# Optimization experiments

Measured on AMD Instinct MI355X. Metric: run time of the kernel, lower is better.

## Reference

```python
import jax, jax.numpy as jnp
import numpy as np

EPS = 1e-7
KERNELS = ((5, 5), (7, 1), (1, 7))
SCALES = (60, 30, 15, 8)


def avg_pool(x, kh, kw):
    # PyTorch AvgPool2d(kernel, stride=1, padding=(kh//2, kw//2)), count_include_pad=True
    s = jax.lax.reduce_window(x, 0.0, jax.lax.add, (1, 1, kh, kw), (1, 1, 1, 1),
                              ((0, 0), (0, 0), (kh // 2, kh // 2), (kw // 2, kw // 2)))
    return s / (kh * kw)


def resize_bilinear(x, oh, ow):
    # F.interpolate(mode='bilinear', align_corners=True), NCHW
    B, C, H, W = x.shape
    def coords(o, s):
        pos = jnp.arange(o) * ((s - 1) / max(o - 1, 1))
        i0 = jnp.floor(pos).astype(jnp.int32)
        i1 = jnp.minimum(i0 + 1, s - 1)
        w = (pos - i0).astype(x.dtype)
        return w, i0, i1
    wy, y0, y1 = coords(oh, H)
    wx, x0, x1 = coords(ow, W)
    rows = x[:, :, y0, :] * (1 - wy)[None, None, :, None] + x[:, :, y1, :] * wy[None, None, :, None]
    return rows[:, :, :, x0] * (1 - wx) + rows[:, :, :, x1] * wx


def setup_inputs() -> dict:
    key = jax.random.key(0)
    ks = jax.random.split(key, 12)
    B, C, H, shot = 2, 1024, 60, 1
    hid, tdim = 256, 300
    return {
        "weight": jax.random.uniform(ks[0], (B, shot, 1, 1), dtype=jnp.float32),
        "query_feat_4": jax.random.normal(ks[1], (B, C, H, H), dtype=jnp.float32),
        "supp_feats": jax.random.normal(ks[2], (shot, B, C, H, H), dtype=jnp.float32),
        "masks": jax.random.uniform(ks[3], (shot, B, 1, 473, 473), dtype=jnp.float32),
        "k": jax.random.normal(ks[4], (B, hid, H, H), dtype=jnp.float32),
        "text": jax.random.normal(ks[5], (B, tdim), dtype=jnp.float32),
        "prototype": jax.random.normal(ks[6], (B, hid, 1, 1), dtype=jnp.float32),
        "w_q": jax.random.normal(ks[7], (tdim + hid, hid), dtype=jnp.float32) * 0.05,
        "w_k": jax.random.normal(ks[8], (hid, hid), dtype=jnp.float32) * 0.05,
        "w_bl": jax.random.normal(ks[9], (hid, hid), dtype=jnp.float32) * 0.05,
        "w_proj": jax.random.normal(ks[10], (hid, hid), dtype=jnp.float32) * 0.05,
        "b_proj": jnp.zeros((hid,), dtype=jnp.float32),
    }


def reference(weight, query_feat_4, supp_feats, masks, k, text, prototype, w_q, w_k, w_bl, w_proj, b_proj):
    # ---------------- SPM: self-activation prior mask ----------------
    B, C, H, W = query_feat_4.shape
    S = H * W
    # pooled query features per kernel (shared across supports)
    q_pooled = []
    for (kh, kw) in KERNELS:
        tq = avg_pool(query_feat_4, kh, kw).reshape(B, C, S)
        tq_t = jnp.transpose(tq, (0, 2, 1))                    # [B,S,C]
        qn = jnp.sqrt((tq_t ** 2).sum(-1, keepdims=True))      # [B,S,1]
        q_pooled.append((tq_t, qn))

    corr_list = []
    for i in range(supp_feats.shape[0]):  # loop over shot (small, fixed)
        tmp_mask = resize_bilinear(masks[i], H, W)
        s = supp_feats[i] * tmp_mask
        region = []
        for (kh, kw), (tq_t, qn) in zip(KERNELS, q_pooled):
            ts = avg_pool(s, kh, kw).reshape(B, C, S)          # [B,C,S]
            sn = jnp.sqrt((ts ** 2).sum(1, keepdims=True))     # [B,1,S]
            sim = jnp.matmul(tq_t, ts) / (jnp.matmul(qn, sn) + EPS) * qn  # [B,S,S]
            sim = sim.mean(2)                                  # [B,S]
            mn = sim.min(1, keepdims=True)
            mx = sim.max(1, keepdims=True)
            sim = (sim - mn) / (mx - mn + EPS)
            region.append(sim.reshape(B, H, W))
        corr_list.append(jnp.stack(region, 1).mean(1))         # [B,H,W]
    corr = jnp.stack(corr_list, 1)                             # [B,shot,H,W]
    corr1 = (weight * corr).sum(1, keepdims=True)              # [B,1,H,W]
    corr2 = resize_bilinear(corr1, SCALES[1], SCALES[1])
    corr3 = resize_bilinear(corr1, SCALES[2], SCALES[2])
    corr4 = resize_bilinear(corr1, SCALES[3], SCALES[3])

    # ---------------- APA: bi-linear cross-modal attention ----------------
    Bk, hid, h, w = k.shape
    proto = prototype.reshape(Bk, 1, hid)                      # [B,1,hid]
    q = jnp.concatenate([text[:, None, :], proto], axis=-1)    # [B,1,embed]
    kx = jnp.einsum('oi,bihw->bohw', w_k, k).reshape(Bk, hid, h * w)
    kx = jnp.transpose(kx, (0, 2, 1))                          # [B,S,hid]
    qx = jnp.einsum('bqe,eh->bqh', q, w_q)                     # [B,1,hid]
    qw = jnp.einsum('bqh,hd->bqd', qx, w_bl)                   # bi_linear score
    score = jnp.einsum('bqd,bsd->bqs', qw, kx)                 # [B,1,S]
    score = jax.nn.softmax(score, axis=-1)
    out = jnp.einsum('bqs,bsd->bqd', score, kx)
    out = jnp.einsum('bqd,do->bqo', out, w_proj) + b_proj      # proj (dropout=eval no-op)
    out = out + proto
    return corr1, corr2, corr3, corr4, out
```

## Files before the change

kernel.cpp:

```cpp
#include <hip/hip_runtime.h>
#include <math.h>

#define EPSF 1e-7f
#define Bsz 2
#define Cch 1024
#define Hh 60
#define Ssz 3600
#define HID 256
#define TDIM 300
#define MH 473

#define TROWS 15
#define LROWS 21
#define LPITCH 68
#define CPG 8

#define OFF_SN2    0
#define OFF_DOT    21600
#define OFF_WMAP   43200
#define OFF_V      64800
#define OFF_NORM   70944
#define OFF_SCORE  92544
#define OFF_KBAR   99744
#define OFF_U      100256

__global__ void __launch_bounds__(256) k_pool_sn2(const float* __restrict__ supp,
                                                  const float* __restrict__ masks,
                                                  const float* __restrict__ text,
                                                  const float* __restrict__ proto,
                                                  const float* __restrict__ w_q,
                                                  const float* __restrict__ w_bl,
                                                  const float* __restrict__ w_k,
                                                  float* __restrict__ ws) {
    __shared__ float  mk[LROWS * LPITCH];
    __shared__ float4 raw[LROWS * LPITCH];
    __shared__ float4 h5s[LROWS * LPITCH];
    int tid = threadIdx.x;
    int tile = blockIdx.x;
    int cg = blockIdx.y;
    int b = blockIdx.z;
    int y0 = tile * TROWS;

    if (cg == 128) {
        if (tile != 0) return;
        char* smem = (char*)raw;
        int lane = tid & 63, wv = tid >> 6;
        float4* p4  = (float4*)smem;
        float*  pf  = (float*)smem;
        float*  xs  = (float*)(smem + 4096);
        float*  qxs = (float*)(smem + 6400);
        float*  qws = (float*)(smem + 7424);
        const float4* wq4  = (const float4*)w_q;
        const float4* wbl4 = (const float4*)w_bl;
        const float4* wk4  = (const float4*)w_k;

        #pragma unroll
        for (int j = 0; j < 3; ++j) {
            int e = tid + 256 * j;
            if (e < TDIM) xs[e] = text[b * TDIM + e];
            else if (e < TDIM + HID) xs[e] = proto[b * HID + e - TDIM];
        }
        __syncthreads();
        float4 acc = {0.f, 0.f, 0.f, 0.f};
        #pragma unroll 4
        for (int j = 0; j < 139; ++j) {
            int e = wv + 4 * j;
            if (e < TDIM + HID) {
                float x = xs[e];
                float4 f = wq4[(size_t)e * 64 + lane];
                acc.x += x * f.x; acc.y += x * f.y; acc.z += x * f.z; acc.w += x * f.w;
            }
        }
        p4[wv * 64 + lane] = acc;
        __syncthreads();
        qxs[tid] = pf[tid] + pf[256 + tid] + pf[512 + tid] + pf[768 + tid];
        __syncthreads();

        acc.x = acc.y = acc.z = acc.w = 0.f;
        #pragma unroll 4
        for (int j = 0; j < 64; ++j) {
            int e = wv + 4 * j;
            float x = qxs[e];
            float4 f = wbl4[(size_t)e * 64 + lane];
            acc.x += x * f.x; acc.y += x * f.y; acc.z += x * f.z; acc.w += x * f.w;
        }
        p4[wv * 64 + lane] = acc;
        __syncthreads();
        qws[tid] = pf[tid] + pf[256 + tid] + pf[512 + tid] + pf[768 + tid];
        __syncthreads();

        acc.x = acc.y = acc.z = acc.w = 0.f;
        #pragma unroll 4
        for (int j = 0; j < 64; ++j) {
            int e = wv + 4 * j;
            float x = qws[e];
            float4 f = wk4[(size_t)e * 64 + lane];
            acc.x += x * f.x; acc.y += x * f.y; acc.z += x * f.z; acc.w += x * f.w;
        }
        p4[wv * 64 + lane] = acc;
        __syncthreads();
        ws[OFF_U + b * HID + tid] = pf[tid] + pf[256 + tid] + pf[512 + tid] + pf[768 + tid];
        return;
    }

    const float4 z4 = {0.f, 0.f, 0.f, 0.f};
    for (int i = tid; i < LROWS * LPITCH; i += 256) {
        mk[i] = 0.f; raw[i] = z4; h5s[i] = z4;
    }
    __syncthreads();

    int lr[5], lx[5]; bool lv[5], la[5];
    #pragma unroll
    for (int j = 0; j < 5; ++j) {
        int idx = tid + 256 * j;
        int r = idx / 60, x = idx - 60 * r;
        lr[j] = r; lx[j] = x;
        la[j] = idx < 1260;
        int iy = y0 - 3 + r;
        lv[j] = la[j] && (iy >= 0) && (iy < Hh);
    }
    #pragma unroll
    for (int j = 0; j < 5; ++j)
        if (lv[j]) {
            int iy = y0 - 3 + lr[j];
            mk[lr[j] * LPITCH + 4 + lx[j]] =
                masks[(size_t)b * MH * MH + (size_t)(iy * 8) * MH + lx[j] * 8];
        }

    int orow[4], ox[4]; bool ov[4];
    #pragma unroll
    for (int j = 0; j < 4; ++j) {
        int o = tid + 256 * j;
        int oy = o / 60, x = o - 60 * oy;
        orow[j] = oy + 3; ox[j] = x; ov[j] = o < 900;
    }
    float a0[4] = {0,0,0,0}, a1[4] = {0,0,0,0}, a2[4] = {0,0,0,0};

    const float* chbase = supp + ((size_t)b * Cch + (size_t)cg * CPG) * Ssz + (y0 - 3) * 60;
    float4 pf[5];
    #pragma unroll
    for (int j = 0; j < 5; ++j) {
        int idx = tid + 256 * j;
        pf[j] = z4;
        if (lv[j]) {
            pf[j].x = chbase[idx];
            pf[j].y = chbase[Ssz + idx];
            pf[j].z = chbase[2 * Ssz + idx];
            pf[j].w = chbase[3 * Ssz + idx];
        }
    }

    for (int p = 0; p < 2; ++p) {
        __syncthreads();
        #pragma unroll
        for (int j = 0; j < 5; ++j)
            if (lv[j]) {
                float m = mk[lr[j] * LPITCH + 4 + lx[j]];
                float4 v = pf[j];
                raw[lr[j] * LPITCH + 4 + lx[j]] =
                    make_float4(v.x * m, v.y * m, v.z * m, v.w * m);
            }
        __syncthreads();
        #pragma unroll
        for (int j = 0; j < 5; ++j)
            if (la[j]) {
                int base = lr[j] * LPITCH + 4 + lx[j];
                float4 m2 = raw[base - 2], m1 = raw[base - 1];
                float4 c0 = raw[base], p1 = raw[base + 1], p2 = raw[base + 2];
                float4 h5;
                h5.x = m2.x + m1.x + c0.x + p1.x + p2.x;
                h5.y = m2.y + m1.y + c0.y + p1.y + p2.y;
                h5.z = m2.z + m1.z + c0.z + p1.z + p2.z;
                h5.w = m2.w + m1.w + c0.w + p1.w + p2.w;
                h5s[base] = h5;
            }
        __syncthreads();
        if (p == 0) {
            const float* nb = chbase + (size_t)4 * Ssz;
            #pragma unroll
            for (int j = 0; j < 5; ++j) {
                int idx = tid + 256 * j;
                pf[j] = z4;
                if (lv[j]) {
                    pf[j].x = nb[idx];
                    pf[j].y = nb[Ssz + idx];
                    pf[j].z = nb[2 * Ssz + idx];
                    pf[j].w = nb[3 * Ssz + idx];
                }
            }
        }
        #pragma unroll
        for (int j = 0; j < 4; ++j)
            if (ov[j]) {
                int base = orow[j] * LPITCH + 4 + ox[j];
                float4 sa = h5s[base - 2*LPITCH], sb = h5s[base - LPITCH], sc0 = h5s[base];
                float4 sd = h5s[base + LPITCH], se = h5s[base + 2*LPITCH];
                float p55x = (sa.x + sb.x + sc0.x + sd.x + se.x) * (1.f / 25.f);
                float p55y = (sa.y + sb.y + sc0.y + sd.y + se.y) * (1.f / 25.f);
                float p55z = (sa.z + sb.z + sc0.z + sd.z + se.z) * (1.f / 25.f);
                float p55w = (sa.w + sb.w + sc0.w + sd.w + se.w) * (1.f / 25.f);
                float4 ra = raw[base - 3*LPITCH], rb = raw[base - 2*LPITCH], rc = raw[base - LPITCH];
                float4 rd = raw[base], re = raw[base + LPITCH], rf = raw[base + 2*LPITCH], rg = raw[base + 3*LPITCH];
                float p71x = (ra.x + rb.x + rc.x + rd.x + re.x + rf.x + rg.x) * (1.f / 7.f);
                float p71y = (ra.y + rb.y + rc.y + rd.y + re.y + rf.y + rg.y) * (1.f / 7.f);
                float p71z = (ra.z + rb.z + rc.z + rd.z + re.z + rf.z + rg.z) * (1.f / 7.f);
                float p71w = (ra.w + rb.w + rc.w + rd.w + re.w + rf.w + rg.w) * (1.f / 7.f);
                float4 m3o = raw[base - 3], p3o = raw[base + 3];
                float p17x = (sc0.x + m3o.x + p3o.x) * (1.f / 7.f);
                float p17y = (sc0.y + m3o.y + p3o.y) * (1.f / 7.f);
                float p17z = (sc0.z + m3o.z + p3o.z) * (1.f / 7.f);
                float p17w = (sc0.w + m3o.w + p3o.w) * (1.f / 7.f);
                a0[j] += p55x * p55x + p55y * p55y + p55z * p55z + p55w * p55w;
                a1[j] += p71x * p71x + p71y * p71y + p71z * p71z + p71w * p71w;
                a2[j] += p17x * p17x + p17y * p17y + p17z * p17z + p17w * p17w;
            }
    }
    float* acc = ws + OFF_SN2 + (size_t)(b * 3) * Ssz;
    #pragma unroll
    for (int j = 0; j < 4; ++j)
        if (ov[j]) {
            int q = (y0 + orow[j] - 3) * 60 + ox[j];
            atomicAdd(&acc[q], a0[j]);
            atomicAdd(&acc[Ssz + q], a1[j]);
            atomicAdd(&acc[2 * Ssz + q], a2[j]);
        }
}

__global__ void __launch_bounds__(1024) k_wmap(const float* __restrict__ masks,
                                               float* __restrict__ ws) {
    __shared__ float inv[LROWS * LPITCH];
    int tile = blockIdx.x;
    int bk = blockIdx.y;
    int b = bk / 3, kt = bk % 3;
    int tid = threadIdx.x;
    int y0 = tile * TROWS;
    for (int i = tid; i < LROWS * LPITCH; i += 1024) inv[i] = 0.f;
    __syncthreads();
    const float* pp = ws + OFF_SN2 + (size_t)bk * Ssz;
    #pragma unroll
    for (int j = 0; j < 2; ++j) {
        int idx = tid + 1024 * j;
        if (idx < 1260) {
            int r = idx / 60, x = idx - 60 * r;
            int iy = y0 - 3 + r;
            if (iy >= 0 && iy < Hh) {
                int q = iy * 60 + x;
                float s = pp[q];
                inv[r * LPITCH + 4 + x] = 1.0f / sqrtf(fmaxf(s, 1e-30f));
            }
        }
    }
    __syncthreads();
    int kh = (kt == 0) ? 5 : (kt == 1) ? 7 : 1;
    int kw = (kt == 0) ? 5 : (kt == 2) ? 7 : 1;
    int rh = kh / 2, rw = kw / 2;
    float norm = 1.f / (float)(kh * kw);
    int o = tid;
    if (o < 900) {
        int oy = o / 60, x = o - 60 * oy;
        int base = (oy + 3) * LPITCH + 4 + x;
        float s = 0.f;
        for (int dy = -rh; dy <= rh; ++dy)
            for (int dx = -rw; dx <= rw; ++dx)
                s += inv[base + dy * LPITCH + dx];
        int gy = y0 + oy;
        float m = masks[(size_t)b * MH * MH + (size_t)(gy * 8) * MH + x * 8];
        ws[OFF_WMAP + (size_t)bk * Ssz + gy * 60 + x] = s * norm * m;
    }
}

__global__ void k_v(const float* __restrict__ supp, float* __restrict__ ws) {
    int cB = blockIdx.x, b = blockIdx.y;
    int tid = threadIdx.x, lane = tid & 63, w = tid >> 6;
    int c0 = cB * 4;
    const float4* sp4 = (const float4*)(supp + ((size_t)b * Cch + c0) * Ssz);
    const float4* w04 = (const float4*)(ws + OFF_WMAP + (size_t)(b * 3 + 0) * Ssz);
    const float4* w14 = (const float4*)(ws + OFF_WMAP + (size_t)(b * 3 + 1) * Ssz);
    const float4* w24 = (const float4*)(ws + OFF_WMAP + (size_t)(b * 3 + 2) * Ssz);
    float a[4][3];
    #pragma unroll
    for (int cc = 0; cc < 4; ++cc) { a[cc][0] = 0; a[cc][1] = 0; a[cc][2] = 0; }
    #pragma unroll
    for (int j = 0; j < 4; ++j) {
        int idx = tid + 256 * j;
        if (idx < 900) {
            float4 g0 = w04[idx], g1 = w14[idx], g2 = w24[idx];
            #pragma unroll
            for (int cc = 0; cc < 4; ++cc) {
                float4 f = sp4[cc * 900 + idx];
                a[cc][0] += f.x * g0.x + f.y * g0.y + f.z * g0.z + f.w * g0.w;
                a[cc][1] += f.x * g1.x + f.y * g1.y + f.z * g1.z + f.w * g1.w;
                a[cc][2] += f.x * g2.x + f.y * g2.y + f.z * g2.z + f.w * g2.w;
            }
        }
    }
    #pragma unroll
    for (int m = 32; m >= 1; m >>= 1)
        #pragma unroll
        for (int cc = 0; cc < 4; ++cc) {
            a[cc][0] += __shfl_xor(a[cc][0], m, 64);
            a[cc][1] += __shfl_xor(a[cc][1], m, 64);
            a[cc][2] += __shfl_xor(a[cc][2], m, 64);
        }
    __shared__ float r[4][3][4];
    if (lane == 0)
        #pragma unroll
        for (int cc = 0; cc < 4; ++cc) {
            r[cc][0][w] = a[cc][0]; r[cc][1][w] = a[cc][1]; r[cc][2][w] = a[cc][2];
        }
    __syncthreads();
    if (tid < 12) {
        int cc = tid / 3, kk = tid - cc * 3;
        float s = r[cc][kk][0] + r[cc][kk][1] + r[cc][kk][2] + r[cc][kk][3];
        ws[OFF_V + (size_t)(b * 3 + kk) * Cch + c0 + cc] = s;
    }
}

__global__ void k_dot(const float* __restrict__ query, float* __restrict__ ws) {
    int qt = blockIdx.x, cc = blockIdx.y, b = blockIdx.z;
    int q = qt * 256 + threadIdx.x;
    if (q >= Ssz) return;
    const float* v0 = ws + OFF_V + (size_t)(b * 3 + 0) * Cch;
    const float* v1 = ws + OFF_V + (size_t)(b * 3 + 1) * Cch;
    const float* v2 = ws + OFF_V + (size_t)(b * 3 + 2) * Cch;
    float a0 = 0, a1 = 0, a2 = 0;
    int c0 = cc * 64;
    #pragma unroll 8
    for (int c = c0; c < c0 + 64; ++c) {
        float qv = query[((size_t)b * Cch + c) * Ssz + q];
        a0 += qv * v0[c]; a1 += qv * v1[c]; a2 += qv * v2[c];
    }
    float* dst = ws + OFF_DOT + (size_t)(b * 3) * Ssz + q;
    atomicAdd(&dst[0], a0);
    atomicAdd(&dst[Ssz], a1);
    atomicAdd(&dst[2 * Ssz], a2);
}

__global__ void __launch_bounds__(1024) k_sim(float* __restrict__ ws) {
    int bkx = blockIdx.x;
    int tid = threadIdx.x;
    int lane = tid & 63, w = tid >> 6;

    __shared__ float sA[66 * LPITCH];
    __shared__ float sB[66 * LPITCH];
    __shared__ float rmin[16], rmax[16];
    int bk = bkx; int b = bk / 3; int kt = bk % 3;

    const float* dp0 = ws + OFF_DOT + (size_t)(b * 3 + kt) * Ssz;
    for (int i = tid; i < 66 * LPITCH; i += 1024) {
        int r = i / LPITCH, col = i - r * LPITCH;
        int y = r - 3, x = col - 4;
        float s = 0.f;
        if (y >= 0 && y < Hh && x >= 0 && x < Hh) {
            s = dp0[y * Hh + x];
        }
        sA[i] = s;
    }
    __syncthreads();
    if (kt != 1) {
        for (int idx = tid; idx < 66 * 60; idx += 1024) {
            int r = idx / 60, x = idx - 60 * r;
            int base = r * LPITCH + 4 + x;
            if (kt == 0)
                sB[base] = sA[base - 2] + sA[base - 1] + sA[base] + sA[base + 1] + sA[base + 2];
            else
                sB[base] = sA[base - 3] + sA[base - 2] + sA[base - 1] + sA[base]
                         + sA[base + 1] + sA[base + 2] + sA[base + 3];
        }
    }
    __syncthreads();
    float norm = ((kt == 0) ? (1.f / 25.f) : (1.f / 7.f)) * (1.f / (float)Ssz);
    float vals[4];
    float vmin = INFINITY, vmax = -INFINITY;
    #pragma unroll
    for (int j = 0; j < 4; ++j) {
        int q = tid + j * 1024;
        if (q < Ssz) {
            int y = q / Hh, x = q - y * Hh;
            int base = (y + 3) * LPITCH + 4 + x;
            float s;
            if (kt == 0)
                s = sB[base - 2*LPITCH] + sB[base - LPITCH] + sB[base]
                  + sB[base + LPITCH] + sB[base + 2*LPITCH];
            else if (kt == 1)
                s = sA[base - 3*LPITCH] + sA[base - 2*LPITCH] + sA[base - LPITCH]
                  + sA[base] + sA[base + LPITCH] + sA[base + 2*LPITCH] + sA[base + 3*LPITCH];
            else
                s = sB[base];
            float val = s * norm;
            vals[j] = val;
            vmin = fminf(vmin, val); vmax = fmaxf(vmax, val);
        }
    }
    #pragma unroll
    for (int m = 32; m >= 1; m >>= 1) {
        vmin = fminf(vmin, __shfl_xor(vmin, m, 64));
        vmax = fmaxf(vmax, __shfl_xor(vmax, m, 64));
    }
    if (lane == 0) { rmin[w] = vmin; rmax[w] = vmax; }
    __syncthreads();
    float mn = rmin[0], mx = rmax[0];
    #pragma unroll
    for (int ww = 1; ww < 16; ++ww) {
        mn = fminf(mn, rmin[ww]); mx = fmaxf(mx, rmax[ww]);
    }
    float inv = 1.f / (mx - mn + EPSF);
    float* np = ws + OFF_NORM + (size_t)(b * 3 + kt) * Ssz;
    #pragma unroll
    for (int j = 0; j < 4; ++j) {
        int q = tid + j * 1024;
        if (q < Ssz) np[q] = (vals[j] - mn) * inv;
    }
}

__global__ void __launch_bounds__(1024)
k_score(const float* __restrict__ kin, const float* __restrict__ weight,
        float* __restrict__ ws, float* __restrict__ out) {
    int st = blockIdx.x, b = blockIdx.y;
    int tid = threadIdx.x;

    if (st == 29) {
        __shared__ float sF[Ssz];
        float wq3 = weight[b] * (1.f / 3.f);
        const float* n0 = ws + OFF_NORM + (size_t)(b * 3 + 0) * Ssz;
        const float* n1 = ws + OFF_NORM + (size_t)(b * 3 + 1) * Ssz;
        const float* n2 = ws + OFF_NORM + (size_t)(b * 3 + 2) * Ssz;
        #pragma unroll
        for (int j = 0; j < 4; ++j) {
            int q = tid + j * 1024;
            if (q < Ssz) {
                float s = n0[q] + n1[q] + n2[q];
                sF[q] = s;
                out[b * Ssz + q] = wq3 * s;
            }
        }
        __syncthreads();
        #pragma unroll
        for (int j = 0; j < 2; ++j) {
            int o = tid + j * 1024;
            if (o >= 1189) continue;
            int O, p, outi;
            if (o < 900)       { O = 30; p = o;        outi = 7200 + b * 900 + p; }
            else if (o < 1125) { O = 15; p = o - 900;  outi = 9000 + b * 225 + p; }
            else               { O = 8;  p = o - 1125; outi = 9450 + b * 64 + p; }
            int y = p / O, x = p - y * O;
            float sc = 59.f / (float)(O - 1);
            float py = y * sc, px = x * sc;
            int y0 = (int)floorf(py), x0 = (int)floorf(px);
            int y1 = min(y0 + 1, 59), x1 = min(x0 + 1, 59);
            float wy = py - y0, wx = px - x0;
            float v = sF[y0 * 60 + x0] * (1.f - wy) * (1.f - wx)
                    + sF[y1 * 60 + x0] * wy * (1.f - wx)
                    + sF[y0 * 60 + x1] * (1.f - wy) * wx
                    + sF[y1 * 60 + x1] * wy * wx;
            out[outi] = wq3 * v;
        }
        return;
    }

    __shared__ float us[HID];
    __shared__ float part[8][128];
    if (tid < HID) us[tid] = ws[OFF_U + b * HID + tid];
    __syncthreads();
    int sl = tid & 127, pt = tid >> 7;
    int s = st * 128 + sl;
    float a = 0.f;
    if (s < Ssz) {
        const float* kb = kin + ((size_t)b * HID + pt * 32) * Ssz + s;
        const float* up = us + pt * 32;
        #pragma unroll
        for (int i = 0; i < 32; ++i) a += up[i] * kb[(size_t)i * Ssz];
    }
    part[pt][sl] = a;
    __syncthreads();
    if (tid < 128 && st * 128 + tid < Ssz) {
        float t = 0.f;
        #pragma unroll
        for (int p = 0; p < 8; ++p) t += part[p][tid];
        ws[OFF_SCORE + (size_t)b * Ssz + st * 128 + tid] = t;
    }
}

__global__ void k_kbar(const float* __restrict__ kin, float* __restrict__ ws) {
    int i = blockIdx.x, b = blockIdx.y;
    int tid = threadIdx.x;
    int lane = tid & 63, w = tid >> 6;
    __shared__ float r1[4], r2[4];
    const float4* s4 = (const float4*)(ws + OFF_SCORE + (size_t)b * Ssz);
    float4 sv[4]; bool act[4];
    float mx = -INFINITY;
    #pragma unroll
    for (int j = 0; j < 4; ++j) {
        int idx = tid + 256 * j;
        act[j] = idx < 900;
        if (act[j]) {
            float4 v = s4[idx];
            sv[j] = v;
            mx = fmaxf(mx, fmaxf(fmaxf(v.x, v.y), fmaxf(v.z, v.w)));
        }
    }
    #pragma unroll
    for (int m = 32; m >= 1; m >>= 1) mx = fmaxf(mx, __shfl_xor(mx, m, 64));
    if (lane == 0) r1[w] = mx;
    __syncthreads();
    mx = fmaxf(fmaxf(r1[0], r1[1]), fmaxf(r1[2], r1[3]));
    __syncthreads();
    const float4* kr = (const float4*)(kin + ((size_t)b * HID + i) * Ssz);
    float se = 0.f, wsum = 0.f;
    #pragma unroll
    for (int j = 0; j < 4; ++j) {
        if (act[j]) {
            int idx = tid + 256 * j;
            float4 v = sv[j];
            float ex = expf(v.x - mx), ey = expf(v.y - mx);
            float ez = expf(v.z - mx), ew = expf(v.w - mx);
            se += ex + ey + ez + ew;
            float4 k4 = kr[idx];
            wsum += ex * k4.x + ey * k4.y + ez * k4.z + ew * k4.w;
        }
    }
    #pragma unroll
    for (int m = 32; m >= 1; m >>= 1) {
        se += __shfl_xor(se, m, 64);
        wsum += __shfl_xor(wsum, m, 64);
    }
    if (lane == 0) { r1[w] = se; r2[w] = wsum; }
    __syncthreads();
    if (tid == 0) {
        float seT = r1[0] + r1[1] + r1[2] + r1[3];
        float wsT = r2[0] + r2[1] + r2[2] + r2[3];
        ws[OFF_KBAR + b * HID + i] = wsT / seT;
    }
}

__global__ void __launch_bounds__(1024, 1)
k_apa_out(const float* __restrict__ w_k, const float* __restrict__ w_proj,
          const float* __restrict__ b_proj, const float* __restrict__ proto,
          const float* __restrict__ ws, float* __restrict__ out) {
    int b = blockIdx.x;
    int tid = threadIdx.x;
    int lane = tid & 63, w = tid >> 6;
    __shared__ float4 kbs[64];
    __shared__ float o1s[256];
    __shared__ float4 p4[16][64];
    const float4* wk4 = (const float4*)w_k;
    const float4* wp4 = (const float4*)w_proj;

    if (tid < 64) kbs[tid] = ((const float4*)(ws + OFF_KBAR + b * HID))[tid];
    __syncthreads();

    float4 kb4 = kbs[lane];
    #pragma unroll
    for (int r = 0; r < 16; ++r) {
        int h = w + 16 * r;
        float4 f = wk4[(size_t)h * 64 + lane];
        float p = f.x * kb4.x + f.y * kb4.y + f.z * kb4.z + f.w * kb4.w;
        #pragma unroll
        for (int m = 32; m >= 1; m >>= 1) p += __shfl_xor(p, m, 64);
        if (lane == 0) o1s[h] = p;
    }
    __syncthreads();

    float4 acc = {0.f, 0.f, 0.f, 0.f};
    #pragma unroll
    for (int j = 0; j < 16; ++j) {
        int d = w + 16 * j;
        float x = o1s[d];
        float4 f = wp4[(size_t)d * 64 + lane];
        acc.x += x * f.x; acc.y += x * f.y; acc.z += x * f.z; acc.w += x * f.w;
    }
    p4[w][lane] = acc;
    __syncthreads();
    if (tid < 256) {
        const float* pf = (const float*)p4;
        float s = 0.f;
        #pragma unroll
        for (int ww = 0; ww < 16; ++ww) s += pf[ww * 256 + tid];
        out[9578 + b * HID + tid] = s + b_proj[tid] + proto[b * HID + tid];
    }
}

extern "C" void kernel_launch(void* const* d_in, const int* in_sizes, int n_in,
                              void* d_out, int out_size, void* d_ws, size_t ws_size,
                              hipStream_t stream) {
    const float* weight = (const float*)d_in[0];
    const float* query  = (const float*)d_in[1];
    const float* supp   = (const float*)d_in[2];
    const float* masks  = (const float*)d_in[3];
    const float* kin    = (const float*)d_in[4];
    const float* text   = (const float*)d_in[5];
    const float* proto  = (const float*)d_in[6];
    const float* w_q    = (const float*)d_in[7];
    const float* w_k    = (const float*)d_in[8];
    const float* w_bl   = (const float*)d_in[9];
    const float* w_proj = (const float*)d_in[10];
    const float* b_proj = (const float*)d_in[11];
    float* out = (float*)d_out;
    float* ws  = (float*)d_ws;

    hipMemsetAsync(ws, 0, (size_t)(2 * 6 * Ssz) * sizeof(float), stream);

    k_pool_sn2<<<dim3(4, 129, 2), 256, 0, stream>>>(supp, masks, text, proto,
                                                    w_q, w_bl, w_k, ws);
    k_wmap<<<dim3(4, 6), 1024, 0, stream>>>(masks, ws);
    k_v<<<dim3(256, 2), 256, 0, stream>>>(supp, ws);
    k_dot<<<dim3(15, 16, 2), 256, 0, stream>>>(query, ws);
    k_sim<<<6, 1024, 0, stream>>>(ws);
    k_score<<<dim3(30, 2), 1024, 0, stream>>>(kin, weight, ws, out);
    k_kbar<<<dim3(HID, 2), 256, 0, stream>>>(kin, ws);
    k_apa_out<<<Bsz, 1024, 0, stream>>>(w_k, w_proj, b_proj, proto, ws, out);
}
```

Baseline: 224.3 us.

## Split serial APA query matvec chain across three kernels with atomic partial sums

The chain of three matrix-vector products (w_q, w_bl, w_k) used to run in one block per batch inside the pool kernel. It is now split across k_pool_sn2, k_wmap and k_v. Each stage is spread over several blocks that write partial sums with atomicAdd into new zeroed workspace slots, so one long serial block no longer sets the pool kernel's tail. The cost is a larger memset, extra atomics, and the qx and qw intermediates passing through global memory between kernels.

```diff
diff --git a/kernel.cpp b/kernel.cpp
--- a/kernel.cpp
+++ b/kernel.cpp
@@ -17,91 +17,43 @@
 
 #define OFF_SN2    0
 #define OFF_DOT    21600
-#define OFF_WMAP   43200
-#define OFF_V      64800
-#define OFF_NORM   70944
-#define OFF_SCORE  92544
-#define OFF_KBAR   99744
-#define OFF_U      100256
+#define OFF_QX     43200
+#define OFF_QW     43712
+#define OFF_U      44224
+#define ZERO_END   44736
+#define OFF_WMAP   44736
+#define OFF_V      66336
+#define OFF_NORM   72480
+#define OFF_SCORE  94080
+#define OFF_KBAR   101280
 
 __global__ void __launch_bounds__(256) k_pool_sn2(const float* __restrict__ supp,
                                                   const float* __restrict__ masks,
                                                   const float* __restrict__ text,
                                                   const float* __restrict__ proto,
                                                   const float* __restrict__ w_q,
-                                                  const float* __restrict__ w_bl,
-                                                  const float* __restrict__ w_k,
                                                   float* __restrict__ ws) {
     __shared__ float  mk[LROWS * LPITCH];
     __shared__ float4 raw[LROWS * LPITCH];
     __shared__ float4 h5s[LROWS * LPITCH];
     int tid = threadIdx.x;
     int tile = blockIdx.x;
-    int cg = blockIdx.y;
     int b = blockIdx.z;
     int y0 = tile * TROWS;
 
-    if (cg == 128) {
-        if (tile != 0) return;
-        char* smem = (char*)raw;
-        int lane = tid & 63, wv = tid >> 6;
-        float4* p4  = (float4*)smem;
-        float*  pf  = (float*)smem;
-        float*  xs  = (float*)(smem + 4096);
-        float*  qxs = (float*)(smem + 6400);
-        float*  qws = (float*)(smem + 7424);
-        const float4* wq4  = (const float4*)w_q;
-        const float4* wbl4 = (const float4*)w_bl;
-        const float4* wk4  = (const float4*)w_k;
-
-        #pragma unroll
-        for (int j = 0; j < 3; ++j) {
-            int e = tid + 256 * j;
-            if (e < TDIM) xs[e] = text[b * TDIM + e];
-            else if (e < TDIM + HID) xs[e] = proto[b * HID + e - TDIM];
-        }
-        __syncthreads();
-        float4 acc = {0.f, 0.f, 0.f, 0.f};
-        #pragma unroll 4
-        for (int j = 0; j < 139; ++j) {
-            int e = wv + 4 * j;
-            if (e < TDIM + HID) {
-                float x = xs[e];
-                float4 f = wq4[(size_t)e * 64 + lane];
-                acc.x += x * f.x; acc.y += x * f.y; acc.z += x * f.z; acc.w += x * f.w;
-            }
-        }
-        p4[wv * 64 + lane] = acc;
-        __syncthreads();
-        qxs[tid] = pf[tid] + pf[256 + tid] + pf[512 + tid] + pf[768 + tid];
-        __syncthreads();
-
-        acc.x = acc.y = acc.z = acc.w = 0.f;
-        #pragma unroll 4
-        for (int j = 0; j < 64; ++j) {
-            int e = wv + 4 * j;
-            float x = qxs[e];
-            float4 f = wbl4[(size_t)e * 64 + lane];
-            acc.x += x * f.x; acc.y += x * f.y; acc.z += x * f.z; acc.w += x * f.w;
-        }
-        p4[wv * 64 + lane] = acc;
-        __syncthreads();
-        qws[tid] = pf[tid] + pf[256 + tid] + pf[512 + tid] + pf[768 + tid];
-        __syncthreads();
-
-        acc.x = acc.y = acc.z = acc.w = 0.f;
-        #pragma unroll 4
-        for (int j = 0; j < 64; ++j) {
-            int e = wv + 4 * j;
-            float x = qws[e];
-            float4 f = wk4[(size_t)e * 64 + lane];
-            acc.x += x * f.x; acc.y += x * f.y; acc.z += x * f.z; acc.w += x * f.w;
-        }
-        p4[wv * 64 + lane] = acc;
-        __syncthreads();
-        ws[OFF_U + b * HID + tid] = pf[tid] + pf[256 + tid] + pf[512 + tid] + pf[768 + tid];
+    if (blockIdx.y == 128) {
+        int e0 = tile * 139;
+        int e1 = (e0 + 139 < TDIM + HID) ? e0 + 139 : TDIM + HID;
+        float s = 0.f;
+        for (int e = e0; e < e1; ++e) {
+            float x = (e < TDIM) ? text[b * TDIM + e] : proto[b * HID + e - TDIM];
+            s += x * w_q[(size_t)e * HID + tid];
+        }
+        atomicAdd(&ws[OFF_QX + b * HID + tid], s);
         return;
     }
+
+    int cg = blockIdx.y;
 
     const float4 z4 = {0.f, 0.f, 0.f, 0.f};
     for (int i = tid; i < LROWS * LPITCH; i += 256) {
@@ -227,12 +179,26 @@
 }
 
 __global__ void __launch_bounds__(1024) k_wmap(const float* __restrict__ masks,
+                                               const float* __restrict__ w_bl,
                                                float* __restrict__ ws) {
     __shared__ float inv[LROWS * LPITCH];
     int tile = blockIdx.x;
+    int tid = threadIdx.x;
+
+    if (blockIdx.y == 6) {
+        int b = tile >> 1, chunk = tile & 1;
+        int h = tid & 255, es = tid >> 8;
+        int e0 = chunk * 128 + es * 32;
+        const float* qx = ws + OFF_QX + b * HID;
+        float s = 0.f;
+        #pragma unroll 8
+        for (int e = e0; e < e0 + 32; ++e) s += qx[e] * w_bl[(size_t)e * HID + h];
+        atomicAdd(&ws[OFF_QW + b * HID + h], s);
+        return;
+    }
+
     int bk = blockIdx.y;
     int b = bk / 3, kt = bk % 3;
-    int tid = threadIdx.x;
     int y0 = tile * TROWS;
     for (int i = tid; i < LROWS * LPITCH; i += 1024) inv[i] = 0.f;
     __syncthreads();
@@ -269,9 +235,22 @@
     }
 }
 
-__global__ void k_v(const float* __restrict__ supp, float* __restrict__ ws) {
+__global__ void k_v(const float* __restrict__ supp, const float* __restrict__ w_k,
+                    float* __restrict__ ws) {
     int cB = blockIdx.x, b = blockIdx.y;
     int tid = threadIdx.x, lane = tid & 63, w = tid >> 6;
+
+    if (cB >= 256) {
+        int chunk = cB - 256;
+        int e0 = chunk * 128;
+        const float* qw = ws + OFF_QW + b * HID;
+        float s = 0.f;
+        #pragma unroll 8
+        for (int e = e0; e < e0 + 128; ++e) s += qw[e] * w_k[(size_t)e * HID + tid];
+        atomicAdd(&ws[OFF_U + b * HID + tid], s);
+        return;
+    }
+
     int c0 = cB * 4;
     const float4* sp4 = (const float4*)(supp + ((size_t)b * Cch + c0) * Ssz);
     const float4* w04 = (const float4*)(ws + OFF_WMAP + (size_t)(b * 3 + 0) * Ssz);
@@ -598,12 +577,11 @@
     float* out = (float*)d_out;
     float* ws  = (float*)d_ws;
 
-    hipMemsetAsync(ws, 0, (size_t)(2 * 6 * Ssz) * sizeof(float), stream);
-
-    k_pool_sn2<<<dim3(4, 129, 2), 256, 0, stream>>>(supp, masks, text, proto,
-                                                    w_q, w_bl, w_k, ws);
-    k_wmap<<<dim3(4, 6), 1024, 0, stream>>>(masks, ws);
-    k_v<<<dim3(256, 2), 256, 0, stream>>>(supp, ws);
+    hipMemsetAsync(ws, 0, (size_t)ZERO_END * sizeof(float), stream);
+
+    k_pool_sn2<<<dim3(4, 129, 2), 256, 0, stream>>>(supp, masks, text, proto, w_q, ws);
+    k_wmap<<<dim3(4, 7), 1024, 0, stream>>>(masks, w_bl, ws);
+    k_v<<<dim3(258, 2), 256, 0, stream>>>(supp, w_k, ws);
     k_dot<<<dim3(15, 16, 2), 256, 0, stream>>>(query, ws);
     k_sim<<<6, 1024, 0, stream>>>(ws);
     k_score<<<dim3(30, 2), 1024, 0, stream>>>(kin, weight, ws, out);
```

Measured after the change: 215.5 us. 1.04x faster.
